# Kernel tuning notes

Measured on AMD Instinct MI355X. Metric: run time of the kernel, lower is better.

The kernel has to match this reference:

```python
import jax, jax.numpy as jnp
import numpy as np

B = 256          # batch
CTX = 512        # context_length
PRED = 64        # prediction_length
H = 512          # hidden size of both GRU layers


def setup_inputs() -> dict:
    key = jax.random.key(0)
    ks = jax.random.split(key, 11)
    s = 0.1  # weight init scale
    f32 = jnp.float32
    return {
        "context": jax.random.normal(ks[0], (B, CTX), f32),
        # GRU layer 0: input_size=1 -> H  (torch gate order: r, z, n)
        "Wih0": jax.random.normal(ks[1], (3 * H, 1), f32) * s,
        "Whh0": jax.random.normal(ks[2], (3 * H, H), f32) * s,
        "bih0": jax.random.normal(ks[3], (3 * H,), f32) * s,
        "bhh0": jax.random.normal(ks[4], (3 * H,), f32) * s,
        # GRU layer 1: H -> H
        "Wih1": jax.random.normal(ks[5], (3 * H, H), f32) * s,
        "Whh1": jax.random.normal(ks[6], (3 * H, H), f32) * s,
        "bih1": jax.random.normal(ks[7], (3 * H,), f32) * s,
        "bhh1": jax.random.normal(ks[8], (3 * H,), f32) * s,
        # Linear head: H -> 1
        "Wout": jax.random.normal(ks[9], (1, H), f32) * s,
        "bout": jax.random.normal(ks[10], (1,), f32) * s,
    }


def _gru_cell(xg, h, Whh, bhh):
    # xg: precomputed input-side gates [B, 3H]; h: [B, H]
    hd = h.shape[-1]
    hg = h @ Whh.T + bhh
    r = jax.nn.sigmoid(xg[:, :hd] + hg[:, :hd])
    z = jax.nn.sigmoid(xg[:, hd:2 * hd] + hg[:, hd:2 * hd])
    n = jnp.tanh(xg[:, 2 * hd:] + r * hg[:, 2 * hd:])
    return (1.0 - z) * n + z * h


def _gru_layer(x, Wih, Whh, bih, bhh):
    # x: [B, L, in] -> outputs [B, L, H], final hidden [B, H]; h0 = zeros (torch default)
    xg = jnp.einsum('bli,gi->blg', x, Wih) + bih  # [B, L, 3H]
    h0 = jnp.zeros((x.shape[0], Whh.shape[1]), x.dtype)

    def step(h, xg_t):
        h2 = _gru_cell(xg_t, h, Whh, bhh)
        return h2, h2

    hT, ys = jax.lax.scan(step, h0, jnp.swapaxes(xg, 0, 1))
    return jnp.swapaxes(ys, 0, 1), hT


def reference(context, Wih0, Whh0, bih0, bhh0, Wih1, Whh1, bih1, bhh1, Wout, bout):
    # scale = |mean(context[:, :context_length])|.clip(1e-5)
    scale = jnp.maximum(jnp.abs(jnp.mean(context[:, :CTX], axis=1, keepdims=True)), 1e-5)  # [B,1]
    x = (context / scale)[..., None]  # [B, CTX, 1]

    # Encoder pass over full context through stacked GRUs
    y0, h0 = _gru_layer(x, Wih0, Whh0, bih0, bhh0)
    y1, h1 = _gru_layer(y0, Wih1, Whh1, bih1, bhh1)

    f0 = (y1[:, -1] @ Wout.T + bout) * scale  # first forecast [B, 1]

    def step(carry, _):
        h0c, h1c, y = carry
        xin = y / scale                       # [B, 1]
        xg0 = xin @ Wih0.T + bih0             # [B, 3H]
        h0n = _gru_cell(xg0, h0c, Whh0, bhh0)
        xg1 = h0n @ Wih1.T + bih1
        h1n = _gru_cell(xg1, h1c, Whh1, bhh1)
        yn = (h1n @ Wout.T + bout) * scale    # [B, 1]
        return (h0n, h1n, yn), yn

    _, ys = jax.lax.scan(step, (h0, h1, f0), None, length=PRED - 1)  # ys: [PRED-1, B, 1]

    rest = jnp.swapaxes(ys[..., 0], 0, 1)  # [B, PRED-1]
    forecast = jnp.concatenate([f0, rest], axis=1)[:, None, :]  # [B, 1, PRED]
    return forecast
```

## Files before the change

kernel.cpp:

```cpp
#include <hip/hip_runtime.h>

typedef unsigned int uint32;
typedef unsigned long long uint64;
typedef _Float16 f16;
typedef _Float16 half8 __attribute__((ext_vector_type(8)));
typedef float floatx4 __attribute__((ext_vector_type(4)));

#define HD    512
#define NBAT  256
#define CTXL  512
#define NPRED 64
#define NBLK  256
#define NTHR  256
#define NSTR  4
#define LDS_BYTES (6*16*64*16)
#define NGEN  575u

__device__ __attribute__((aligned(256))) f16   g_h0[4][NSTR][32][64][16];
__device__ __attribute__((aligned(256))) f16   g_h1[2][NSTR][32][64][16];
__device__ __attribute__((aligned(256))) float g_yacc[NPRED][NBAT];
__device__ __attribute__((aligned(256))) float g_scale[NBAT];
__device__ __attribute__((aligned(256))) uint32 g_alines[NSTR*16*32];
__device__ __attribute__((aligned(256))) uint32 g_blines[NSTR*16*32];
__device__ __attribute__((aligned(256))) uint32 g_ilines[NSTR*16*32];
__device__ __attribute__((aligned(256))) uint32 g_sepoch[NSTR*64];

__device__ __forceinline__ float sigm(float x){ return 1.f/(1.f+__expf(-x)); }
__device__ __forceinline__ float tanh_(float x){ return 1.f - 2.f/(__expf(2.f*x)+1.f); }

__device__ __forceinline__ uint32 ld_u32_dc(const uint32* p){
  return __hip_atomic_load(p, __ATOMIC_RELAXED, __HIP_MEMORY_SCOPE_AGENT);
}
__device__ __forceinline__ void st_u32_dc(uint32* p, uint32 v){
  __hip_atomic_store(p, v, __ATOMIC_RELAXED, __HIP_MEMORY_SCOPE_AGENT);
}
__device__ __forceinline__ void st_u64_dc(uint64* p, uint64 v){
  __hip_atomic_store(p, v, __ATOMIC_RELAXED, __HIP_MEMORY_SCOPE_AGENT);
}
__device__ __forceinline__ float ld_f32_dc(const float* p){
  return __hip_atomic_load(p, __ATOMIC_RELAXED, __HIP_MEMORY_SCOPE_AGENT);
}
__device__ __forceinline__ void st_f32_dc(float* p, float v){
  __hip_atomic_store(p, v, __ATOMIC_RELAXED, __HIP_MEMORY_SCOPE_AGENT);
}
__device__ __forceinline__ float ld_f16_dc(const f16* p){
  unsigned short u = __hip_atomic_load((const unsigned short*)p, __ATOMIC_RELAXED, __HIP_MEMORY_SCOPE_AGENT);
  union { unsigned short u; f16 h; } c; c.u = u; return (float)c.h;
}
__device__ __forceinline__ void st_f16_dc(f16* p, f16 h){
  union { unsigned short u; f16 h; } c; c.h = h;
  __hip_atomic_store((unsigned short*)p, c.u, __ATOMIC_RELAXED, __HIP_MEMORY_SCOPE_AGENT);
}
__device__ __forceinline__ half8 ld_half8_dc(const f16* p){
  const uint64* q = (const uint64*)p;
  union { uint64 u[2]; half8 h; } r;
  r.u[0] = __hip_atomic_load(q+0, __ATOMIC_RELAXED, __HIP_MEMORY_SCOPE_AGENT);
  r.u[1] = __hip_atomic_load(q+1, __ATOMIC_RELAXED, __HIP_MEMORY_SCOPE_AGENT);
  return r.h;
}

__device__ __forceinline__ void waitl(const uint32* lines, uint32 tgt){
  if (threadIdx.x < 64) {
    const int lane = threadIdx.x;
    const uint32* fp = &lines[(lane & 15)*32];
    for (;;) {
      bool ok = (lane >= 16) || ((int)(ld_u32_dc(fp) - tgt) >= 0);
      if (__ballot(ok) == ~0ull) break;
      __builtin_amdgcn_s_sleep(1);
    }
  }
  __syncthreads();
}
__device__ __forceinline__ void arrive(uint32* lines, int li){
  __builtin_amdgcn_fence(__ATOMIC_RELEASE, "workgroup");
  __syncthreads();
  if (threadIdx.x == 0)
    __hip_atomic_fetch_add(&lines[li*32], 1u, __ATOMIC_RELAXED, __HIP_MEMORY_SCOPE_AGENT);
}
__device__ __forceinline__ void arrive_rel(uint32* lines, int li){
  __builtin_amdgcn_fence(__ATOMIC_RELEASE, "workgroup");
  __syncthreads();
  if (threadIdx.x == 0)
    __hip_atomic_fetch_add(&lines[li*32], 1u, __ATOMIC_RELEASE, __HIP_MEMORY_SCOPE_AGENT);
}

__global__ __launch_bounds__(NTHR, 1) void rnn_persist(
    const float* __restrict__ ctx,
    const float* __restrict__ Wih0,
    const float* __restrict__ Whh0,
    const float* __restrict__ bih0,
    const float* __restrict__ bhh0,
    const float* __restrict__ Wih1,
    const float* __restrict__ Whh1,
    const float* __restrict__ bih1,
    const float* __restrict__ bhh1,
    const float* __restrict__ Wout,
    const float* __restrict__ boutp,
    float* __restrict__ out)
{
  extern __shared__ char smem_raw[];
  f16* wlds = (f16*)smem_raw;
  __shared__ float wsum[4];

  const int tid  = threadIdx.x;
  const int bid  = blockIdx.x;
  const int sid  = bid >> 6;
  const int rr_  = bid & 63;
  const bool isA = rr_ < 32;
  const int ng   = isA ? rr_ : rr_ - 32;
  const int Mbase = sid * 64;
  const int s0    = ng * 16;
  const int w    = tid >> 6;
  const int lane = tid & 63;
  const int quad = lane >> 4;
  const int l16  = lane & 15;

  uint32* al = &g_alines[sid*512];
  uint32* bl = &g_blines[sid*512];
  uint32* il = &g_ilines[sid*512];
  const uint32 E = ld_u32_dc(&g_sepoch[sid*64]);
  const uint32 baseA = E * (2u*NGEN);
  const uint32 baseB = E * (2u*NGEN);

  {
    const int b = bid;
    float s2 = 0.f;
    for (int k = tid; k < CTXL; k += NTHR) s2 += ctx[b*CTXL + k];
    #pragma unroll
    for (int m = 1; m < 64; m <<= 1) s2 += __shfl_xor(s2, m, 64);
    if (lane == 0) wsum[w] = s2;
    __syncthreads();
    float tot = wsum[0] + wsum[1] + wsum[2] + wsum[3];
    float sc  = fmaxf(fabsf(tot / (float)CTXL), 1e-5f);
    if (tid == 0) st_f32_dc(&g_scale[b], sc);
    uint64* z0 = (uint64*)&g_h0[3][sid][0][0][0];
    uint64* z1 = (uint64*)&g_h1[0][sid][0][0][0];
    uint64* z2 = (uint64*)&g_h1[1][sid][0][0][0];
    const int off = rr_*128;
    for (int k = tid; k < 128; k += NTHR) {
      st_u64_dc(z0+off+k, 0ull); st_u64_dc(z1+off+k, 0ull); st_u64_dc(z2+off+k, 0ull);
    }
    if (tid < 64) st_f32_dc(&g_yacc[rr_][Mbase + tid], 0.f);
  }

  {
    const int nfrag = isA ? (3*16*64) : (6*16*64);
    for (int idx = tid; idx < nfrag; idx += NTHR) {
      const int ln = idx & 63;
      const int kc = (idx >> 6) & 15;
      const int mg = idx >> 10;
      const float* Wsrc;
      int g;
      if (isA)            { Wsrc = Whh0; g = mg; }
      else if (mg < 3)    { Wsrc = Wih1; g = mg; }
      else                { Wsrc = Whh1; g = mg - 3; }
      const float* src = Wsrc + (size_t)(g*HD + s0 + (ln & 15))*HD + (ln >> 4)*8 + kc*32;
      f16* dst = wlds + (size_t)idx*8;
      #pragma unroll
      for (int j = 0; j < 8; ++j) dst[j] = (f16)src[j];
    }
  }

  float wi_r=0, wi_z=0, wi_n=0, bi_r, bi_z, bi_n, bh_r, bh_z, bh_n;
  float woutj=0, boutv=0;
  const int jcol = s0 + l16;
  const int mf = w;
  if (isA) {
    wi_r = Wih0[jcol]; wi_z = Wih0[HD + jcol]; wi_n = Wih0[2*HD + jcol];
    bi_r = bih0[jcol]; bi_z = bih0[HD + jcol]; bi_n = bih0[2*HD + jcol];
    bh_r = bhh0[jcol]; bh_z = bhh0[HD + jcol]; bh_n = bhh0[2*HD + jcol];
  } else {
    bi_r = bih1[jcol]; bi_z = bih1[HD + jcol]; bi_n = bih1[2*HD + jcol];
    bh_r = bhh1[jcol]; bh_z = bhh1[HD + jcol]; bh_n = bhh1[2*HD + jcol];
    woutj = Wout[jcol]; boutv = boutp[0];
  }

  const int rl0 = mf*16 + quad*4;
  const int arl = mf*16 + l16;
  const int own = ng*1024;
  const size_t afrag = (size_t)(quad>>1)*1024 + (size_t)arl*16 + (quad&1)*8;

  arrive_rel(il, rr_ & 15);
  waitl(il, E*4u + 4u);
  __builtin_amdgcn_fence(__ATOMIC_ACQUIRE, "agent");
  __syncthreads();

  float scl[4];
  {
    const int bb = Mbase + rl0;
    #pragma unroll
    for (int reg = 0; reg < 4; ++reg) scl[reg] = ld_f32_dc(&g_scale[bb + reg]);
  }

  float chk = 0.f;
  float hold[4] = {0.f, 0.f, 0.f, 0.f};

  if (isA) {
    for (int sA = 0; sA < (int)NGEN; ++sA) {
      const int b0 = Mbase + rl0;
      float xv[4];
      if (sA < 512) {
        #pragma unroll
        for (int reg = 0; reg < 4; ++reg)
          xv[reg] = ctx[(b0+reg)*CTXL + sA] / scl[reg];
      }
      waitl(al, baseA + 2u*(uint32)sA);
      const f16* hrd = &g_h0[(sA+3)&3][sid][0][0][0];
      f16*       hwr = &g_h0[ sA   &3][sid][0][0][0];
      const f16* aptr = hrd + afrag;
      half8 av[16];
      #pragma unroll
      for (int kc = 0; kc < 16; ++kc) av[kc] = ld_half8_dc(aptr + kc*2048);
      if (sA < 512) {
        if (sA >= 4) waitl(bl, baseB + 2u*(uint32)(sA-3));
      } else {
        waitl(bl, baseB + 2u*(uint32)sA);
        #pragma unroll
        for (int reg = 0; reg < 4; ++reg)
          xv[reg] = ld_f32_dc(&g_yacc[sA-512][b0+reg]);
      }
      floatx4 ar = {0.f,0.f,0.f,0.f}, az = ar, an_ = ar;
      const f16* fb = wlds + (size_t)lane*8;
      #pragma unroll
      for (int kc = 0; kc < 16; ++kc) {
        const f16* fkc = fb + (size_t)kc*512;
        half8 v;
        v = *(const half8*)(fkc);          ar  = __builtin_amdgcn_mfma_f32_16x16x32_f16(av[kc], v, ar,  0,0,0);
        v = *(const half8*)(fkc + 8192);   az  = __builtin_amdgcn_mfma_f32_16x16x32_f16(av[kc], v, az,  0,0,0);
        v = *(const half8*)(fkc + 16384);  an_ = __builtin_amdgcn_mfma_f32_16x16x32_f16(av[kc], v, an_, 0,0,0);
      }
      #pragma unroll
      for (int reg = 0; reg < 4; ++reg) {
        float hgr = ar[reg] + bh_r, hgz = az[reg] + bh_z, hgn = an_[reg] + bh_n;
        float rg  = sigm(fmaf(xv[reg], wi_r, bi_r) + hgr);
        float zg  = sigm(fmaf(xv[reg], wi_z, bi_z) + hgz);
        float ng_ = tanh_(fmaf(xv[reg], wi_n, bi_n) + rg*hgn);
        f16 hq = (f16)((1.f - zg)*ng_ + zg*hold[reg]);
        st_f16_dc(&hwr[own + (rl0+reg)*16 + l16], hq);
        hold[reg] = (float)hq;
      }
      #pragma unroll
      for (int reg = 0; reg < 4; ++reg)
        chk += ld_f16_dc(&hwr[own + (rl0+reg)*16 + l16]);
      arrive(al, rr_ & 15);
    }
  } else {
    for (int sB = 0; sB < (int)NGEN; ++sB) {
      waitl(al, baseA + 2u*(uint32)(sB+1));
      const f16* h0rd = &g_h0[sB&3][sid][0][0][0];
      const f16* a0p = h0rd + afrag;
      half8 a0v[16];
      #pragma unroll
      for (int kc = 0; kc < 16; ++kc) a0v[kc] = ld_half8_dc(a0p + kc*2048);
      waitl(bl, baseB + 2u*(uint32)sB);
      const f16* h1rd = &g_h1[ sB   &1][sid][0][0][0];
      f16*       h1wr = &g_h1[(sB+1)&1][sid][0][0][0];
      const int b0 = Mbase + rl0;
      const f16* a1p = h1rd + afrag;
      half8 a1v[16];
      #pragma unroll
      for (int kc = 0; kc < 16; ++kc) a1v[kc] = ld_half8_dc(a1p + kc*2048);
      floatx4 xr = {0.f,0.f,0.f,0.f}, xz = xr, xn = xr, hr = xr, hz = xr, hn = xr;
      const f16* fb = wlds + (size_t)lane*8;
      #pragma unroll
      for (int kc = 0; kc < 16; ++kc) {
        const f16* fkc = fb + (size_t)kc*512;
        half8 v;
        v = *(const half8*)(fkc);           xr = __builtin_amdgcn_mfma_f32_16x16x32_f16(a0v[kc], v, xr, 0,0,0);
        v = *(const half8*)(fkc + 8192);    xz = __builtin_amdgcn_mfma_f32_16x16x32_f16(a0v[kc], v, xz, 0,0,0);
        v = *(const half8*)(fkc + 16384);   xn = __builtin_amdgcn_mfma_f32_16x16x32_f16(a0v[kc], v, xn, 0,0,0);
      }
      #pragma unroll
      for (int kc = 0; kc < 16; ++kc) {
        const f16* fkc = fb + (size_t)kc*512;
        half8 v;
        v = *(const half8*)(fkc + 24576);   hr = __builtin_amdgcn_mfma_f32_16x16x32_f16(a1v[kc], v, hr, 0,0,0);
        v = *(const half8*)(fkc + 32768);   hz = __builtin_amdgcn_mfma_f32_16x16x32_f16(a1v[kc], v, hz, 0,0,0);
        v = *(const half8*)(fkc + 40960);   hn = __builtin_amdgcn_mfma_f32_16x16x32_f16(a1v[kc], v, hn, 0,0,0);
      }
      #pragma unroll
      for (int reg = 0; reg < 4; ++reg) {
        const int b = b0 + reg;
        float rg  = sigm(xr[reg] + bi_r + hr[reg] + bh_r);
        float zg  = sigm(xz[reg] + bi_z + hz[reg] + bh_z);
        float ng_ = tanh_(xn[reg] + bi_n + rg*(hn[reg] + bh_n));
        float hnew = (1.f - zg)*ng_ + zg*hold[reg];
        f16 hq = (f16)hnew;
        st_f16_dc(&h1wr[own + (rl0+reg)*16 + l16], hq);
        hold[reg] = (float)hq;
        if (sB >= 511) {
          float c = hnew * woutj;
          c += __shfl_xor(c, 1, 64); c += __shfl_xor(c, 2, 64);
          c += __shfl_xor(c, 4, 64); c += __shfl_xor(c, 8, 64);
          if (l16 == 0) {
            if (ng == 0) c += boutv;
            float old = __hip_atomic_fetch_add(&g_yacc[sB-511][b], c,
                          __ATOMIC_RELAXED, __HIP_MEMORY_SCOPE_AGENT);
            chk += old;
          }
        }
      }
      #pragma unroll
      for (int reg = 0; reg < 4; ++reg)
        chk += ld_f16_dc(&h1wr[own + (rl0+reg)*16 + l16]);
      arrive(bl, ng & 15);
    }
  }

  if (chk == -1.25e38f) st_f32_dc(&g_scale[0], 0.f);

  waitl(bl, baseB + 2u*NGEN);
  if (tid < 64) {
    const int b = Mbase + tid;
    out[b*NPRED + rr_] = ld_f32_dc(&g_yacc[rr_][b]) * ld_f32_dc(&g_scale[b]);
  }
  if (rr_ == 0) {
    waitl(al, baseA + 2u*NGEN);
    if (tid == 0) st_u32_dc(&g_sepoch[sid*64], E + 1u);
  }
}

extern "C" void kernel_launch(void* const* d_in, const int* in_sizes, int n_in,
                              void* d_out, int out_size, void* d_ws, size_t ws_size,
                              hipStream_t stream) {
  const float* ctx   = (const float*)d_in[0];
  const float* Wih0  = (const float*)d_in[1];
  const float* Whh0  = (const float*)d_in[2];
  const float* bih0  = (const float*)d_in[3];
  const float* bhh0  = (const float*)d_in[4];
  const float* Wih1  = (const float*)d_in[5];
  const float* Whh1  = (const float*)d_in[6];
  const float* bih1  = (const float*)d_in[7];
  const float* bhh1  = (const float*)d_in[8];
  const float* Wout  = (const float*)d_in[9];
  const float* boutp = (const float*)d_in[10];
  float* out = (float*)d_out;

  hipFuncSetAttribute(reinterpret_cast<const void*>(rnn_persist),
                      hipFuncAttributeMaxDynamicSharedMemorySize, LDS_BYTES);

  void* params[] = {
    (void*)&ctx, (void*)&Wih0, (void*)&Whh0, (void*)&bih0, (void*)&bhh0,
    (void*)&Wih1, (void*)&Whh1, (void*)&bih1, (void*)&bhh1,
    (void*)&Wout, (void*)&boutp, (void*)&out
  };
  hipLaunchCooperativeKernel(reinterpret_cast<void*>(rnn_persist),
                             dim3(NBLK), dim3(NTHR), params, LDS_BYTES, stream);
}
```

Baseline: 3.855 ms.

## Store every hidden-state step in its own buffer to drop WAR waits

```diff
diff --git a/kernel.cpp b/kernel.cpp
--- a/kernel.cpp
+++ b/kernel.cpp
@@ -16,8 +16,8 @@
 #define LDS_BYTES (6*16*64*16)
 #define NGEN  575u
 
-__device__ __attribute__((aligned(256))) f16   g_h0[4][NSTR][32][64][16];
-__device__ __attribute__((aligned(256))) f16   g_h1[2][NSTR][32][64][16];
+__device__ __attribute__((aligned(256))) f16   g_h0s[NGEN+2][NSTR][32][64][16];
+__device__ __attribute__((aligned(256))) f16   g_h1s[NGEN+2][NSTR][32][64][16];
 __device__ __attribute__((aligned(256))) float g_yacc[NPRED][NBAT];
 __device__ __attribute__((aligned(256))) float g_scale[NBAT];
 __device__ __attribute__((aligned(256))) uint32 g_alines[NSTR*16*32];
@@ -51,13 +51,11 @@
   union { unsigned short u; f16 h; } c; c.h = h;
   __hip_atomic_store((unsigned short*)p, c.u, __ATOMIC_RELAXED, __HIP_MEMORY_SCOPE_AGENT);
 }
-__device__ __forceinline__ half8 ld_half8_dc(const f16* p){
-  const uint64* q = (const uint64*)p;
-  union { uint64 u[2]; half8 h; } r;
-  r.u[0] = __hip_atomic_load(q+0, __ATOMIC_RELAXED, __HIP_MEMORY_SCOPE_AGENT);
-  r.u[1] = __hip_atomic_load(q+1, __ATOMIC_RELAXED, __HIP_MEMORY_SCOPE_AGENT);
-  return r.h;
-}
+__device__ __forceinline__ void ld_b128_sc0(floatx4* d, const f16* p){
+  asm volatile("global_load_dwordx4 %0, %1, off sc0" : "=v"(*d) : "v"(p));
+}
+#define VM_DRAIN() do { asm volatile("s_waitcnt vmcnt(0)":::"memory"); \
+                        __builtin_amdgcn_sched_barrier(0); } while(0)
 
 __device__ __forceinline__ void waitl(const uint32* lines, uint32 tgt){
   if (threadIdx.x < 64) {
@@ -133,12 +131,11 @@
     float tot = wsum[0] + wsum[1] + wsum[2] + wsum[3];
     float sc  = fmaxf(fabsf(tot / (float)CTXL), 1e-5f);
     if (tid == 0) st_f32_dc(&g_scale[b], sc);
-    uint64* z0 = (uint64*)&g_h0[3][sid][0][0][0];
-    uint64* z1 = (uint64*)&g_h1[0][sid][0][0][0];
-    uint64* z2 = (uint64*)&g_h1[1][sid][0][0][0];
+    uint64* z0 = (uint64*)&g_h0s[0][sid][0][0][0];
+    uint64* z1 = (uint64*)&g_h1s[0][sid][0][0][0];
     const int off = rr_*128;
     for (int k = tid; k < 128; k += NTHR) {
-      st_u64_dc(z0+off+k, 0ull); st_u64_dc(z1+off+k, 0ull); st_u64_dc(z2+off+k, 0ull);
+      st_u64_dc(z0+off+k, 0ull); st_u64_dc(z1+off+k, 0ull);
     }
     if (tid < 64) st_f32_dc(&g_yacc[rr_][Mbase + tid], 0.f);
   }
@@ -179,6 +176,7 @@
   const int arl = mf*16 + l16;
   const int own = ng*1024;
   const size_t afrag = (size_t)(quad>>1)*1024 + (size_t)arl*16 + (quad&1)*8;
+  const size_t SSTEP = (size_t)NSTR*32*64*16;
 
   arrive_rel(il, rr_ & 15);
   waitl(il, E*4u + 4u);
@@ -196,6 +194,7 @@
   float hold[4] = {0.f, 0.f, 0.f, 0.f};
 
   if (isA) {
+    const f16* h0base = &g_h0s[0][sid][0][0][0];
     for (int sA = 0; sA < (int)NGEN; ++sA) {
       const int b0 = Mbase + rl0;
       float xv[4];
@@ -205,29 +204,29 @@
           xv[reg] = ctx[(b0+reg)*CTXL + sA] / scl[reg];
       }
       waitl(al, baseA + 2u*(uint32)sA);
-      const f16* hrd = &g_h0[(sA+3)&3][sid][0][0][0];
-      f16*       hwr = &g_h0[ sA   &3][sid][0][0][0];
+      const f16* hrd = h0base + (size_t)sA*SSTEP;
+      f16*       hwr = (f16*)h0base + (size_t)(sA+1)*SSTEP;
       const f16* aptr = hrd + afrag;
-      half8 av[16];
-      #pragma unroll
-      for (int kc = 0; kc < 16; ++kc) av[kc] = ld_half8_dc(aptr + kc*2048);
-      if (sA < 512) {
-        if (sA >= 4) waitl(bl, baseB + 2u*(uint32)(sA-3));
-      } else {
+      union { floatx4 f; half8 h; } av[16];
+      #pragma unroll
+      for (int kc = 0; kc < 16; ++kc)
+        ld_b128_sc0(&av[kc].f, aptr + kc*2048);
+      if (sA >= 512) {
         waitl(bl, baseB + 2u*(uint32)sA);
         #pragma unroll
         for (int reg = 0; reg < 4; ++reg)
           xv[reg] = ld_f32_dc(&g_yacc[sA-512][b0+reg]);
       }
+      VM_DRAIN();
       floatx4 ar = {0.f,0.f,0.f,0.f}, az = ar, an_ = ar;
       const f16* fb = wlds + (size_t)lane*8;
       #pragma unroll
       for (int kc = 0; kc < 16; ++kc) {
         const f16* fkc = fb + (size_t)kc*512;
         half8 v;
-        v = *(const half8*)(fkc);          ar  = __builtin_amdgcn_mfma_f32_16x16x32_f16(av[kc], v, ar,  0,0,0);
-        v = *(const half8*)(fkc + 8192);   az  = __builtin_amdgcn_mfma_f32_16x16x32_f16(av[kc], v, az,  0,0,0);
-        v = *(const half8*)(fkc + 16384);  an_ = __builtin_amdgcn_mfma_f32_16x16x32_f16(av[kc], v, an_, 0,0,0);
+        v = *(const half8*)(fkc);          ar  = __builtin_amdgcn_mfma_f32_16x16x32_f16(av[kc].h, v, ar,  0,0,0);
+        v = *(const half8*)(fkc + 8192);   az  = __builtin_amdgcn_mfma_f32_16x16x32_f16(av[kc].h, v, az,  0,0,0);
+        v = *(const half8*)(fkc + 16384);  an_ = __builtin_amdgcn_mfma_f32_16x16x32_f16(av[kc].h, v, an_, 0,0,0);
       }
       #pragma unroll
       for (int reg = 0; reg < 4; ++reg) {
@@ -245,38 +244,40 @@
       arrive(al, rr_ & 15);
     }
   } else {
+    const f16* h0base = &g_h0s[0][sid][0][0][0];
+    const f16* h1base = &g_h1s[0][sid][0][0][0];
     for (int sB = 0; sB < (int)NGEN; ++sB) {
       waitl(al, baseA + 2u*(uint32)(sB+1));
-      const f16* h0rd = &g_h0[sB&3][sid][0][0][0];
-      const f16* a0p = h0rd + afrag;
-      half8 a0v[16];
-      #pragma unroll
-      for (int kc = 0; kc < 16; ++kc) a0v[kc] = ld_half8_dc(a0p + kc*2048);
+      const f16* a0p = h0base + (size_t)(sB+1)*SSTEP + afrag;
+      union { floatx4 f; half8 h; } a0v[16], a1v[16];
+      #pragma unroll
+      for (int kc = 0; kc < 16; ++kc)
+        ld_b128_sc0(&a0v[kc].f, a0p + kc*2048);
       waitl(bl, baseB + 2u*(uint32)sB);
-      const f16* h1rd = &g_h1[ sB   &1][sid][0][0][0];
-      f16*       h1wr = &g_h1[(sB+1)&1][sid][0][0][0];
+      const f16* a1p = h1base + (size_t)sB*SSTEP + afrag;
+      f16*       h1wr = (f16*)h1base + (size_t)(sB+1)*SSTEP;
       const int b0 = Mbase + rl0;
-      const f16* a1p = h1rd + afrag;
-      half8 a1v[16];
-      #pragma unroll
-      for (int kc = 0; kc < 16; ++kc) a1v[kc] = ld_half8_dc(a1p + kc*2048);
+      #pragma unroll
+      for (int kc = 0; kc < 16; ++kc)
+        ld_b128_sc0(&a1v[kc].f, a1p + kc*2048);
+      VM_DRAIN();
       floatx4 xr = {0.f,0.f,0.f,0.f}, xz = xr, xn = xr, hr = xr, hz = xr, hn = xr;
       const f16* fb = wlds + (size_t)lane*8;
       #pragma unroll
       for (int kc = 0; kc < 16; ++kc) {
         const f16* fkc = fb + (size_t)kc*512;
         half8 v;
-        v = *(const half8*)(fkc);           xr = __builtin_amdgcn_mfma_f32_16x16x32_f16(a0v[kc], v, xr, 0,0,0);
-        v = *(const half8*)(fkc + 8192);    xz = __builtin_amdgcn_mfma_f32_16x16x32_f16(a0v[kc], v, xz, 0,0,0);
-        v = *(const half8*)(fkc + 16384);   xn = __builtin_amdgcn_mfma_f32_16x16x32_f16(a0v[kc], v, xn, 0,0,0);
+        v = *(const half8*)(fkc);           xr = __builtin_amdgcn_mfma_f32_16x16x32_f16(a0v[kc].h, v, xr, 0,0,0);
+        v = *(const half8*)(fkc + 8192);    xz = __builtin_amdgcn_mfma_f32_16x16x32_f16(a0v[kc].h, v, xz, 0,0,0);
+        v = *(const half8*)(fkc + 16384);   xn = __builtin_amdgcn_mfma_f32_16x16x32_f16(a0v[kc].h, v, xn, 0,0,0);
       }
       #pragma unroll
       for (int kc = 0; kc < 16; ++kc) {
         const f16* fkc = fb + (size_t)kc*512;
         half8 v;
-        v = *(const half8*)(fkc + 24576);   hr = __builtin_amdgcn_mfma_f32_16x16x32_f16(a1v[kc], v, hr, 0,0,0);
-        v = *(const half8*)(fkc + 32768);   hz = __builtin_amdgcn_mfma_f32_16x16x32_f16(a1v[kc], v, hz, 0,0,0);
-        v = *(const half8*)(fkc + 40960);   hn = __builtin_amdgcn_mfma_f32_16x16x32_f16(a1v[kc], v, hn, 0,0,0);
+        v = *(const half8*)(fkc + 24576);   hr = __builtin_amdgcn_mfma_f32_16x16x32_f16(a1v[kc].h, v, hr, 0,0,0);
+        v = *(const half8*)(fkc + 32768);   hz = __builtin_amdgcn_mfma_f32_16x16x32_f16(a1v[kc].h, v, hz, 0,0,0);
+        v = *(const half8*)(fkc + 40960);   hn = __builtin_amdgcn_mfma_f32_16x16x32_f16(a1v[kc].h, v, hn, 0,0,0);
       }
       #pragma unroll
       for (int reg = 0; reg < 4; ++reg) {
```

Result: faster. 3.571 ms (median of 4 runs) (-7.4%).
